# Kernel optimization log

Measured on AMD Instinct MI355X. Metric: run time of the kernel, lower is better.

The kernel has to match this reference:

```python
import jax, jax.numpy as jnp
import numpy as np

TOPK, NUM_CLASSES = 13, 80
ALPHA, BETA, GAMMA, EPS = 1.0, 5.0, 3.0, 1e-09


def _make_boxes(key, shape, img=640.0, wmin=10.0, wmax=120.0):
    k1, k2 = jax.random.split(key)
    cxy = jax.random.uniform(k1, shape[:-1] + (2,), minval=0.0, maxval=img)
    wh = jax.random.uniform(k2, shape[:-1] + (2,), minval=wmin, maxval=wmax)
    return jnp.concatenate([cxy - wh / 2, cxy + wh / 2], axis=-1)


def setup_inputs() -> dict:
    key = jax.random.key(0)
    ks = jax.random.split(key, 7)
    bs, A, C, n = 16, 8400, 80, 60
    return {
        'pd_scores': jax.random.uniform(ks[0], (bs, A, C), dtype=jnp.float32),
        'pd_bboxes': _make_boxes(ks[1], (bs, A, 4)),
        'pd_angles': jax.random.uniform(ks[2], (bs, A, 1), minval=0.0, maxval=90.0),
        'anc_points': jax.random.uniform(ks[3], (A, 2), minval=0.0, maxval=640.0),
        'gt_labels': jax.random.randint(ks[4], (bs, n, 1), 0, C, dtype=jnp.int32),
        'gt_bboxes': _make_boxes(ks[5], (bs, n, 4)),
        'gt_angles': jax.random.uniform(ks[6], (bs, n, 1), minval=0.0, maxval=90.0),
        'mask_gt': jnp.ones((bs, n, 1), jnp.float32),
        'epoch_num': 1,
    }


def _cos_fn(x, ar, beta=2.0):
    return 0.5 + 0.5 * jnp.cos(beta / ar * x / 180.0 * jnp.pi + jnp.pi * (1.0 - beta / (2.0 * ar)))


def _angle_measure(pd_angles, gt_angles, gt_bboxes):
    # gt area ratio w/h -> (bs, n, 1, 1)
    w = gt_bboxes[..., 2:3] - gt_bboxes[..., 0:1]
    h = gt_bboxes[..., 3:4] - gt_bboxes[..., 1:2]
    ar = (w / (h + 1e-05))[:, :, None, :]
    theta = jnp.abs(gt_angles[:, :, None, :] - pd_angles[:, None, :, :])  # (bs,n,A,1)
    av = 1.0 / ar / (2.0 - 1.0 / ar)
    mx = _cos_fn(0.0, ar)
    mn = _cos_fn(90.0, ar)
    r = (_cos_fn(theta, ar) - mn) / (mx - mn) * (1.0 - av) + av
    r = jnp.where(jnp.isnan(r), 0.0, r)
    return jnp.squeeze(r, -1)  # (bs, n, A)


def _pairwise_iou(gt, pd):
    # gt (bs,n,4), pd (bs,A,4) -> (bs,n,A)
    lt = jnp.maximum(gt[:, :, None, :2], pd[:, None, :, :2])
    rb = jnp.minimum(gt[:, :, None, 2:], pd[:, None, :, 2:])
    inter = jnp.clip(rb - lt, 0.0).prod(-1)
    a1 = jnp.clip(gt[..., 2:] - gt[..., :2], 0.0).prod(-1)[:, :, None]
    a2 = jnp.clip(pd[..., 2:] - pd[..., :2], 0.0).prod(-1)[:, None, :]
    return inter / (a1 + a2 - inter + EPS)


def _select_topk(metrics, topk_mask):
    bs, n, A = metrics.shape
    _, idxs = jax.lax.top_k(metrics, TOPK)
    idxs = jnp.where(topk_mask, idxs, 0)
    flat = idxs.reshape(bs * n, TOPK)
    cnt = jnp.zeros((bs * n, A), jnp.int32).at[jnp.arange(bs * n)[:, None], flat].add(1)
    cnt = cnt.reshape(bs, n, A)
    return jnp.where(cnt > 1, 0, cnt).astype(metrics.dtype)


def _select_highest_overlaps(mask_pos, overlaps, n):
    fg = mask_pos.sum(-2)                                   # (bs, A)
    multi = fg[:, None, :] > 1                              # (bs, 1, A)
    is_max = jax.nn.one_hot(overlaps.argmax(1), n, axis=1, dtype=mask_pos.dtype)  # (bs,n,A)
    mask_pos = jnp.where(multi, is_max, mask_pos)
    fg = mask_pos.sum(-2)
    tgt_idx = mask_pos.argmax(-2)                           # (bs, A)
    return tgt_idx, fg, mask_pos


def reference(pd_scores, pd_bboxes, pd_angles, anc_points, gt_labels, gt_bboxes, gt_angles, mask_gt, epoch_num):
    bs, A, C = pd_scores.shape
    n = gt_bboxes.shape[1]
    lab = gt_labels[..., 0].astype(jnp.int32)               # (bs, n)

    # bbox_scores: pd_scores[b, :, gt_label] -> (bs, n, A)
    pts = jnp.transpose(pd_scores, (0, 2, 1))               # (bs, C, A)
    bbox_scores = jnp.take_along_axis(pts, lab[:, :, None], axis=1)

    overlaps = _pairwise_iou(gt_bboxes, pd_bboxes)          # (bs, n, A)
    ang = _angle_measure(pd_angles, gt_angles, gt_bboxes)   # (bs, n, A)
    align = bbox_scores ** ALPHA * overlaps ** BETA * ang ** GAMMA

    # anchors-inside-gt mask (bs, n, A)
    lt = anc_points[None, None, :, :] - gt_bboxes[:, :, None, :2]
    rb = gt_bboxes[:, :, None, 2:] - anc_points[None, None, :, :]
    in_gts = (jnp.concatenate([lt, rb], -1).min(-1) > EPS).astype(align.dtype)

    topk_mask = jnp.broadcast_to(mask_gt > 0, (bs, n, TOPK))
    mask_topk = _select_topk(align * in_gts, topk_mask)
    mask_pos = mask_topk * in_gts * mask_gt                 # (bs, n, A)

    tgt_idx, fg, mask_pos = _select_highest_overlaps(mask_pos, overlaps, n)

    # gather per-anchor targets from flattened gt tensors
    off = tgt_idx + jnp.arange(bs, dtype=tgt_idx.dtype)[:, None] * n   # (bs, A)
    tlab = lab.reshape(-1)[off]
    tlab = jnp.where(tlab < 0, 0, tlab)
    tbb = gt_bboxes.reshape(-1, 4)[off]                     # (bs, A, 4)
    tang = gt_angles.reshape(-1, 1)[off]                    # (bs, A, 1)
    ts = jax.nn.one_hot(tlab, C, dtype=pd_scores.dtype)     # (bs, A, C)
    ts = jnp.where(fg[:, :, None] > 0, ts, 0.0)

    # normalized alignment metric scaling
    align = align * mask_pos
    pam = align.max(-1, keepdims=True)                      # (bs, n, 1)
    pov = (overlaps * mask_pos).max(-1, keepdims=True)      # (bs, n, 1)
    norm = (align * pov / (pam + EPS)).max(-2)[:, :, None]  # (bs, A, 1)
    ts = ts * norm

    return tlab, tbb, tang, ts, fg > 0
```

## Files before the change

### kernel.cpp

```cpp
#include <hip/hip_runtime.h>
#include <math.h>

#define TOPK 13
#define PI_F 3.14159265358979323846f
#define K1_THREADS 256
#define K1_WAVES (K1_THREADS / 64)

typedef unsigned int u32;
typedef unsigned long long u64;

__device__ __forceinline__ u32 ford(float f) {
    u32 u = __float_as_uint(f);
    return (u & 0x80000000u) ? ~u : (u | 0x80000000u);
}
__device__ __forceinline__ float funord(u32 o) {
    u32 u = (o & 0x80000000u) ? (o & 0x7FFFFFFFu) : ~o;
    return __uint_as_float(u);
}

__device__ __forceinline__ float iou_fn(float4 g, float4 p) {
    float ltx = fmaxf(g.x, p.x), lty = fmaxf(g.y, p.y);
    float rbx = fminf(g.z, p.z), rby = fminf(g.w, p.w);
    float inter = fmaxf(rbx - ltx, 0.0f) * fmaxf(rby - lty, 0.0f);
    float a1 = fmaxf(g.z - g.x, 0.0f) * fmaxf(g.w - g.y, 0.0f);
    float a2 = fmaxf(p.z - p.x, 0.0f) * fmaxf(p.w - p.y, 0.0f);
    return inter / (((a1 + a2) - inter) + 1e-9f);
}

struct RowParams { float av, bar, offc, mx, mn; };

__device__ __forceinline__ RowParams row_params(float4 g) {
    float w = g.z - g.x, h = g.w - g.y;
    float ar = w / (h + 1e-5f);
    float ia = 1.0f / ar;
    RowParams rp;
    rp.av = ia / (2.0f - ia);
    rp.bar = 2.0f / ar;
    rp.offc = PI_F * (1.0f - 2.0f / (2.0f * ar));
    rp.mx = 0.5f + 0.5f * cosf(rp.offc);
    rp.mn = 0.5f + 0.5f * cosf(rp.bar * 90.0f / 180.0f * PI_F + rp.offc);
    return rp;
}

__device__ __forceinline__ float ang_measure(const RowParams& rp, float theta) {
    float cfv = 0.5f + 0.5f * cosf(rp.bar * theta / 180.0f * PI_F + rp.offc);
    float r = (cfv - rp.mn) / (rp.mx - rp.mn) * (1.0f - rp.av) + rp.av;
    return isnan(r) ? 0.0f : r;
}

__device__ __forceinline__ float align_fn(float s, float iou, float r) {
    float iou2 = iou * iou;
    float iou5 = (iou2 * iou2) * iou;
    float r3 = (r * r) * r;
    return (s * iou5) * r3;
}

__global__ void k0_init(int* cnt, int* assign1, u32* pam, u32* pov, int BA, int BN) {
    int t = blockIdx.x * blockDim.x + threadIdx.x;
    if (t < BA) { cnt[t] = 0; assign1[t] = -1; }
    if (t < BN) { pam[t] = 0x80000000u; pov[t] = 0x80000000u; }
}

__global__ __launch_bounds__(K1_THREADS)
void k1_topk(const float* __restrict__ scores, const float* __restrict__ pbox,
             const float* __restrict__ pang, const float* __restrict__ anc,
             const int* __restrict__ glab, const float* __restrict__ gbox,
             const float* __restrict__ gang, const float* __restrict__ mgt,
             int* __restrict__ cnt, int* __restrict__ assign1,
             int bs, int A, int n, int C) {
    int j = blockIdx.x;
    int b = j % bs;
    int i = j / bs;
    int bi = b * n + i;
    int tid = threadIdx.x;

    float mg = mgt[bi];
    if (!(mg > 0.0f)) return;

    float4 g = ((const float4*)gbox)[bi];
    int lab = glab[bi];
    float ga = gang[bi];
    RowParams rp = row_params(g);

    const float4* pb = ((const float4*)pbox) + (size_t)b * A;
    const float* pa = pang + (size_t)b * A;
    const float2* ac = (const float2*)anc;
    const float* sc = scores + (size_t)b * A * C + lab;

    u64 arr[TOPK];
#pragma unroll
    for (int jj = 0; jj < TOPK; jj++) arr[jj] = 0ull;
    u64 zkey = 0ull;

    for (int a = tid; a < A; a += K1_THREADS) {
        float4 p = pb[a];
        float pav = pa[a];
        float2 apt = ac[a];
        float iou = iou_fn(g, p);
        float mnv = fminf(fminf(apt.x - g.x, apt.y - g.y), fminf(g.z - apt.x, g.w - apt.y));
        bool needAlign = (mnv > 1e-9f) && (iou > 0.0f);
        if (needAlign || zkey == 0ull) {
            float th = fabsf(ga - pav);
            float r = ang_measure(rp, th);
            bool zeroCand;
            if (needAlign && r > 0.0f) {
                float s = sc[(size_t)a * C];
                float v = align_fn(s, iou, r);
                if (v > 0.0f) {
                    zeroCand = false;
                    u64 key = ((u64)ford(v) << 32) | (u64)(0xFFFFFFFFu - (u32)a);
                    if (key > arr[TOPK - 1]) {
#pragma unroll
                        for (int jj = 0; jj < TOPK; jj++) {
                            u64 hi = arr[jj] > key ? arr[jj] : key;
                            u64 lo = arr[jj] > key ? key : arr[jj];
                            arr[jj] = hi;
                            key = lo;
                        }
                    }
                } else {
                    zeroCand = true;
                }
            } else {
                zeroCand = (r >= 0.0f);
            }
            if (zeroCand && zkey == 0ull) {
                zkey = (0x80000000ull << 32) | (u64)(0xFFFFFFFFu - (u32)a);
            }
        }
    }
    if (zkey > arr[TOPK - 1]) {
        u64 key = zkey;
#pragma unroll
        for (int jj = 0; jj < TOPK; jj++) {
            u64 hi = arr[jj] > key ? arr[jj] : key;
            u64 lo = arr[jj] > key ? key : arr[jj];
            arr[jj] = hi;
            key = lo;
        }
    }

    __shared__ u64 wtop[K1_WAVES * TOPK];
    int lane = tid & 63, wv = tid >> 6;
    for (int round = 0; round < TOPK; round++) {
        u64 m = arr[0];
#pragma unroll
        for (int st = 32; st > 0; st >>= 1) {
            u64 o = __shfl_xor(m, st, 64);
            if (o > m) m = o;
        }
        if (lane == 0) wtop[wv * TOPK + round] = m;
        if (arr[0] == m && m != 0ull) {
#pragma unroll
            for (int jj = 0; jj < TOPK - 1; jj++) arr[jj] = arr[jj + 1];
            arr[TOPK - 1] = 0ull;
        }
    }
    __syncthreads();

    if (wv == 0) {
        const int NK = K1_WAVES * TOPK;
        u64 ka = (lane < NK) ? wtop[lane] : 0ull;
        for (int round = 0; round < TOPK; round++) {
            u64 m = ka;
#pragma unroll
            for (int st = 32; st > 0; st >>= 1) {
                u64 o = __shfl_xor(m, st, 64);
                if (o > m) m = o;
            }
            if (m == 0ull) break;
            if (ka == m) {
                ka = 0ull;
                int a = (int)(0xFFFFFFFFu - (u32)(m & 0xFFFFFFFFull));
                float2 apt = ac[a];
                float mnv = fminf(fminf(apt.x - g.x, apt.y - g.y),
                                  fminf(g.z - apt.x, g.w - apt.y));
                if (mnv > 1e-9f) {
                    atomicAdd(&cnt[(size_t)b * A + a], 1);
                    atomicMax(&assign1[(size_t)b * A + a], i);
                }
            }
        }
    }
}

__global__ __launch_bounds__(256)
void k2_resolve(const float* __restrict__ scores, const float* __restrict__ pbox,
                const float* __restrict__ pang, const int* __restrict__ glab,
                const float* __restrict__ gbox, const float* __restrict__ gang,
                const int* __restrict__ cnt, const int* __restrict__ assign1,
                int* __restrict__ assign, float* __restrict__ alignv,
                u32* __restrict__ pam, u32* __restrict__ pov,
                int bs, int A, int n, int C) {
    int t = blockIdx.x * blockDim.x + threadIdx.x;
    if (t >= bs * A) return;
    int b = t / A;
    int c = cnt[t];
    int asg = -1;
    float alv = 0.0f;
    if (c > 0) {
        float4 p = ((const float4*)pbox)[t];
        if (c == 1) {
            asg = assign1[t];
        } else {
            float best = -1.0f;
            asg = 0;
            for (int i = 0; i < n; i++) {
                float4 gi = ((const float4*)gbox)[b * n + i];
                float io = iou_fn(gi, p);
                if (io > best) { best = io; asg = i; }
            }
        }
        float4 g = ((const float4*)gbox)[b * n + asg];
        RowParams rp = row_params(g);
        float iou = iou_fn(g, p);
        float th = fabsf(gang[b * n + asg] - pang[t]);
        float r = ang_measure(rp, th);
        float s = scores[(size_t)t * C + glab[b * n + asg]];
        alv = align_fn(s, iou, r);
        atomicMax(&pam[b * n + asg], ford(alv));
        atomicMax(&pov[b * n + asg], ford(iou));
    }
    assign[t] = asg;
    alignv[t] = alv;
}

__global__ __launch_bounds__(256)
void k3_out(const int* __restrict__ glab, const float* __restrict__ gbox,
            const float* __restrict__ gang, const int* __restrict__ assign,
            const float* __restrict__ alignv, const u32* __restrict__ pam,
            const u32* __restrict__ pov, float* __restrict__ out,
            int bs, int A, int n, int C) {
    __shared__ float s_nv[256];
    __shared__ int s_lf[256];
    int tid = threadIdx.x;
    int base = blockIdx.x * 256;
    int t = base + tid;
    int BA = bs * A;

    if (t < BA) {
        int b = t / A;
        int asg = assign[t];
        bool fg = asg >= 0;
        int tgt = fg ? asg : 0;
        int lb = glab[b * n + tgt];
        if (lb < 0) lb = 0;

        float* o_tlab = out;
        float* o_tbb = out + BA;
        float* o_tang = out + (size_t)BA * 5;
        float* o_fg = out + (size_t)BA * 6 + (size_t)BA * C;

        o_tlab[t] = (float)lb;
        ((float4*)o_tbb)[t] = ((const float4*)gbox)[b * n + tgt];
        o_tang[t] = gang[b * n + tgt];
        o_fg[t] = fg ? 1.0f : 0.0f;

        float nv = 0.0f;
        if (fg) {
            float pamv = funord(pam[b * n + asg]);
            float povv = funord(pov[b * n + asg]);
            float vv = (alignv[t] * povv) / (pamv + 1e-9f);
            nv = fmaxf(vv, 0.0f);
        }
        s_nv[tid] = nv;
        s_lf[tid] = fg ? lb : -1;
    } else {
        s_nv[tid] = 0.0f;
        s_lf[tid] = -1;
    }
    __syncthreads();

    int Q = C / 4;
    int nA = min(256, BA - base);
    if (nA <= 0) return;
    int total = nA * Q;
    float4* o_ts = (float4*)(out + (size_t)BA * 6) + (size_t)base * Q;
    for (int idx = tid; idx < total; idx += 256) {
        int tl = idx / Q;
        int q = idx - tl * Q;
        float nv = s_nv[tl];
        int lf = s_lf[tl];
        int cb = q * 4;
        float4 o;
        o.x = (lf == cb) ? nv : 0.0f;
        o.y = (lf == cb + 1) ? nv : 0.0f;
        o.z = (lf == cb + 2) ? nv : 0.0f;
        o.w = (lf == cb + 3) ? nv : 0.0f;
        o_ts[idx] = o;
    }
}

extern "C" void kernel_launch(void* const* d_in, const int* in_sizes, int n_in,
                              void* d_out, int out_size, void* d_ws, size_t ws_size,
                              hipStream_t stream) {
    const float* scores = (const float*)d_in[0];
    const float* pbox = (const float*)d_in[1];
    const float* pang = (const float*)d_in[2];
    const float* anc = (const float*)d_in[3];
    const int* glab = (const int*)d_in[4];
    const float* gbox = (const float*)d_in[5];
    const float* gang = (const float*)d_in[6];
    const float* mgt = (const float*)d_in[7];

    const int C = 80;
    int A = in_sizes[3] / 2;
    int bs = in_sizes[0] / (A * C);
    int n = in_sizes[4] / bs;
    int BA = bs * A;
    int BN = bs * n;

    char* ws = (char*)d_ws;
    int* cnt = (int*)ws;        ws += sizeof(int) * (size_t)BA;
    int* assign1 = (int*)ws;    ws += sizeof(int) * (size_t)BA;
    int* assign = (int*)ws;     ws += sizeof(int) * (size_t)BA;
    float* alignv = (float*)ws; ws += sizeof(float) * (size_t)BA;
    u32* pam = (u32*)ws;        ws += sizeof(u32) * (size_t)BN;
    u32* pov = (u32*)ws;        ws += sizeof(u32) * (size_t)BN;

    k0_init<<<(BA + 255) / 256, 256, 0, stream>>>(cnt, assign1, pam, pov, BA, BN);
    k1_topk<<<BN, K1_THREADS, 0, stream>>>(scores, pbox, pang, anc, glab, gbox, gang, mgt,
                                           cnt, assign1, bs, A, n, C);
    k2_resolve<<<(BA + 255) / 256, 256, 0, stream>>>(scores, pbox, pang, glab, gbox, gang,
                                                     cnt, assign1, assign, alignv, pam, pov,
                                                     bs, A, n, C);
    k3_out<<<(BA + 255) / 256, 256, 0, stream>>>(glab, gbox, gang, assign, alignv, pam, pov,
                                                 (float*)d_out, bs, A, n, C);
}
```

Baseline: 170.0 us.

## Split top-k scan into contiguous anchor chunks with separate merge kernel

The per-gt top-k kernel now gives each wavefront a contiguous chunk of anchors (8 chunks, 2 blocks per gt row) instead of striding 256 threads over all anchors. Each wave writes its top-13 list to workspace, and a new 64-thread merge kernel picks the global top-13 and does the atomics. The scan loop also software-prefetches the next anchor's box, angle, anchor point and score. It keeps up to two zero-score candidates per lane so the zero-fill tie-breaking still works after chunking. The cost is an extra kernel launch and a workspace round trip in exchange for more blocks in flight and better memory-latency hiding.

```diff
diff --git a/kernel.cpp b/kernel.cpp
--- a/kernel.cpp
+++ b/kernel.cpp
@@ -3,8 +3,8 @@
 
 #define TOPK 13
 #define PI_F 3.14159265358979323846f
-#define K1_THREADS 256
-#define K1_WAVES (K1_THREADS / 64)
+#define K1_CHUNKS 8
+#define K1_CPB 4
 
 typedef unsigned int u32;
 typedef unsigned long long u64;
@@ -55,27 +55,42 @@
     return (s * iou5) * r3;
 }
 
+__device__ __forceinline__ void insert13(u64* arr, u64 key) {
+    if (key > arr[TOPK - 1]) {
+#pragma unroll
+        for (int jj = 0; jj < TOPK; jj++) {
+            u64 hi = arr[jj] > key ? arr[jj] : key;
+            u64 lo = arr[jj] > key ? key : arr[jj];
+            arr[jj] = hi;
+            key = lo;
+        }
+    }
+}
+
 __global__ void k0_init(int* cnt, int* assign1, u32* pam, u32* pov, int BA, int BN) {
     int t = blockIdx.x * blockDim.x + threadIdx.x;
     if (t < BA) { cnt[t] = 0; assign1[t] = -1; }
     if (t < BN) { pam[t] = 0x80000000u; pov[t] = 0x80000000u; }
 }
 
-__global__ __launch_bounds__(K1_THREADS)
+__global__ __launch_bounds__(256)
 void k1_topk(const float* __restrict__ scores, const float* __restrict__ pbox,
              const float* __restrict__ pang, const float* __restrict__ anc,
              const int* __restrict__ glab, const float* __restrict__ gbox,
              const float* __restrict__ gang, const float* __restrict__ mgt,
-             int* __restrict__ cnt, int* __restrict__ assign1,
+             u64* __restrict__ wslist,
              int bs, int A, int n, int C) {
     int j = blockIdx.x;
     int b = j % bs;
-    int i = j / bs;
+    int r2 = j / bs;
+    int i = r2 % n;
+    int cg = r2 / n;
     int bi = b * n + i;
     int tid = threadIdx.x;
-
-    float mg = mgt[bi];
-    if (!(mg > 0.0f)) return;
+    int lane = tid & 63, wv = tid >> 6;
+    int chunk = cg * K1_CPB + wv;
+
+    if (!(mgt[bi] > 0.0f)) return;
 
     float4 g = ((const float4*)gbox)[bi];
     int lab = glab[bi];
@@ -87,61 +102,69 @@
     const float2* ac = (const float2*)anc;
     const float* sc = scores + (size_t)b * A * C + lab;
 
+    int CS = (A + K1_CHUNKS - 1) / K1_CHUNKS;
+    int start = chunk * CS;
+    int end = min(start + CS, A);
+    int clampA = end - 1;
+
     u64 arr[TOPK];
 #pragma unroll
     for (int jj = 0; jj < TOPK; jj++) arr[jj] = 0ull;
-    u64 zkey = 0ull;
-
-    for (int a = tid; a < A; a += K1_THREADS) {
-        float4 p = pb[a];
-        float pav = pa[a];
-        float2 apt = ac[a];
+    u64 zk0 = 0ull, zk1 = 0ull;
+
+    int a = start + lane;
+    int ca = min(a, clampA);
+    float4 p = pb[ca];
+    float pav = pa[ca];
+    float2 apt = ac[ca];
+    float mnv = fminf(fminf(apt.x - g.x, apt.y - g.y), fminf(g.z - apt.x, g.w - apt.y));
+    bool inG = (mnv > 1e-9f) && (a < end);
+    float s = 0.0f;
+    if (inG) s = sc[(size_t)ca * C];
+
+    int nit = (end - start + 63) >> 6;
+    for (int it = 0; it < nit; ++it) {
+        int an = a + 64;
+        int can = min(an, clampA);
+        float4 p2 = pb[can];
+        float pav2 = pa[can];
+        float2 apt2 = ac[can];
+        float mnv2 = fminf(fminf(apt2.x - g.x, apt2.y - g.y),
+                           fminf(g.z - apt2.x, g.w - apt2.y));
+        bool inG2 = (mnv2 > 1e-9f) && (an < end);
+        float s2 = 0.0f;
+        if (inG2) s2 = sc[(size_t)can * C];
+
         float iou = iou_fn(g, p);
-        float mnv = fminf(fminf(apt.x - g.x, apt.y - g.y), fminf(g.z - apt.x, g.w - apt.y));
-        bool needAlign = (mnv > 1e-9f) && (iou > 0.0f);
-        if (needAlign || zkey == 0ull) {
+        bool needAlign = inG && (iou > 0.0f);
+        bool valid = a < end;
+        if (needAlign || (zk1 == 0ull && valid)) {
             float th = fabsf(ga - pav);
             float r = ang_measure(rp, th);
             bool zeroCand;
             if (needAlign && r > 0.0f) {
-                float s = sc[(size_t)a * C];
                 float v = align_fn(s, iou, r);
                 if (v > 0.0f) {
                     zeroCand = false;
-                    u64 key = ((u64)ford(v) << 32) | (u64)(0xFFFFFFFFu - (u32)a);
-                    if (key > arr[TOPK - 1]) {
-#pragma unroll
-                        for (int jj = 0; jj < TOPK; jj++) {
-                            u64 hi = arr[jj] > key ? arr[jj] : key;
-                            u64 lo = arr[jj] > key ? key : arr[jj];
-                            arr[jj] = hi;
-                            key = lo;
-                        }
-                    }
+                    insert13(arr, ((u64)ford(v) << 32) | (u64)(0xFFFFFFFFu - (u32)a));
                 } else {
                     zeroCand = true;
                 }
             } else {
                 zeroCand = (r >= 0.0f);
             }
-            if (zeroCand && zkey == 0ull) {
-                zkey = (0x80000000ull << 32) | (u64)(0xFFFFFFFFu - (u32)a);
+            if (zeroCand) {
+                u64 kz = (0x80000000ull << 32) | (u64)(0xFFFFFFFFu - (u32)a);
+                if (zk0 == 0ull) zk0 = kz;
+                else if (zk1 == 0ull) zk1 = kz;
             }
         }
-    }
-    if (zkey > arr[TOPK - 1]) {
-        u64 key = zkey;
-#pragma unroll
-        for (int jj = 0; jj < TOPK; jj++) {
-            u64 hi = arr[jj] > key ? arr[jj] : key;
-            u64 lo = arr[jj] > key ? key : arr[jj];
-            arr[jj] = hi;
-            key = lo;
-        }
-    }
-
-    __shared__ u64 wtop[K1_WAVES * TOPK];
-    int lane = tid & 63, wv = tid >> 6;
+        a = an; p = p2; pav = pav2; mnv = mnv2; inG = inG2; s = s2;
+    }
+    insert13(arr, zk0);
+    insert13(arr, zk1);
+
+    u64* dst = wslist + ((size_t)bi * K1_CHUNKS + chunk) * TOPK;
     for (int round = 0; round < TOPK; round++) {
         u64 m = arr[0];
 #pragma unroll
@@ -149,36 +172,54 @@
             u64 o = __shfl_xor(m, st, 64);
             if (o > m) m = o;
         }
-        if (lane == 0) wtop[wv * TOPK + round] = m;
+        if (lane == 0) dst[round] = m;
         if (arr[0] == m && m != 0ull) {
 #pragma unroll
             for (int jj = 0; jj < TOPK - 1; jj++) arr[jj] = arr[jj + 1];
             arr[TOPK - 1] = 0ull;
         }
     }
-    __syncthreads();
-
-    if (wv == 0) {
-        const int NK = K1_WAVES * TOPK;
-        u64 ka = (lane < NK) ? wtop[lane] : 0ull;
-        for (int round = 0; round < TOPK; round++) {
-            u64 m = ka;
-#pragma unroll
-            for (int st = 32; st > 0; st >>= 1) {
-                u64 o = __shfl_xor(m, st, 64);
-                if (o > m) m = o;
-            }
-            if (m == 0ull) break;
-            if (ka == m) {
-                ka = 0ull;
-                int a = (int)(0xFFFFFFFFu - (u32)(m & 0xFFFFFFFFull));
-                float2 apt = ac[a];
-                float mnv = fminf(fminf(apt.x - g.x, apt.y - g.y),
-                                  fminf(g.z - apt.x, g.w - apt.y));
-                if (mnv > 1e-9f) {
-                    atomicAdd(&cnt[(size_t)b * A + a], 1);
-                    atomicMax(&assign1[(size_t)b * A + a], i);
-                }
+}
+
+__global__ __launch_bounds__(64)
+void k1m_merge(const float* __restrict__ anc, const float* __restrict__ gbox,
+               const float* __restrict__ mgt, const u64* __restrict__ wslist,
+               int* __restrict__ cnt, int* __restrict__ assign1,
+               int bs, int A, int n) {
+    int j = blockIdx.x;
+    int b = j % bs;
+    int i = j / bs;
+    int bi = b * n + i;
+    if (!(mgt[bi] > 0.0f)) return;
+    int lane = threadIdx.x;
+
+    const int NK = K1_CHUNKS * TOPK;
+    const u64* src = wslist + (size_t)bi * NK;
+    u64 ka = src[lane];
+    u64 kb = (lane + 64 < NK) ? src[lane + 64] : 0ull;
+
+    float4 g = ((const float4*)gbox)[bi];
+    const float2* ac = (const float2*)anc;
+
+    for (int round = 0; round < TOPK; round++) {
+        u64 m = ka > kb ? ka : kb;
+#pragma unroll
+        for (int st = 32; st > 0; st >>= 1) {
+            u64 o = __shfl_xor(m, st, 64);
+            if (o > m) m = o;
+        }
+        if (m == 0ull) break;
+        bool own = false;
+        if (ka == m) { ka = 0ull; own = true; }
+        else if (kb == m) { kb = 0ull; own = true; }
+        if (own) {
+            int aa = (int)(0xFFFFFFFFu - (u32)(m & 0xFFFFFFFFull));
+            float2 apt = ac[aa];
+            float mnv = fminf(fminf(apt.x - g.x, apt.y - g.y),
+                              fminf(g.z - apt.x, g.w - apt.y));
+            if (mnv > 1e-9f) {
+                atomicAdd(&cnt[(size_t)b * A + aa], 1);
+                atomicMax(&assign1[(size_t)b * A + aa], i);
             }
         }
     }
@@ -311,6 +352,7 @@
     int BN = bs * n;
 
     char* ws = (char*)d_ws;
+    u64* wslist = (u64*)ws;     ws += sizeof(u64) * (size_t)BN * K1_CHUNKS * TOPK;
     int* cnt = (int*)ws;        ws += sizeof(int) * (size_t)BA;
     int* assign1 = (int*)ws;    ws += sizeof(int) * (size_t)BA;
     int* assign = (int*)ws;     ws += sizeof(int) * (size_t)BA;
@@ -319,8 +361,10 @@
     u32* pov = (u32*)ws;        ws += sizeof(u32) * (size_t)BN;
 
     k0_init<<<(BA + 255) / 256, 256, 0, stream>>>(cnt, assign1, pam, pov, BA, BN);
-    k1_topk<<<BN, K1_THREADS, 0, stream>>>(scores, pbox, pang, anc, glab, gbox, gang, mgt,
-                                           cnt, assign1, bs, A, n, C);
+    k1_topk<<<BN * (K1_CHUNKS / K1_CPB), 256, 0, stream>>>(scores, pbox, pang, anc, glab,
+                                                           gbox, gang, mgt, wslist,
+                                                           bs, A, n, C);
+    k1m_merge<<<BN, 64, 0, stream>>>(anc, gbox, mgt, wslist, cnt, assign1, bs, A, n);
     k2_resolve<<<(BA + 255) / 256, 256, 0, stream>>>(scores, pbox, pang, glab, gbox, gang,
                                                      cnt, assign1, assign, alignv, pam, pov,
                                                      bs, A, n, C);
```

Result: slower. 186.9 us (+9.9%).

## Zero the one-hot target buffer inside the top-k kernel and prefetch anchors

Applied to the files above, without the earlier changes.

The large zero-fill of the (bs, A, C) target-score output moves into the top-k kernel. Each block clears its chunk interleaved with its anchor loop, so the memory-bound stores overlap the compute-bound scan. The output kernel then writes only the single nonzero entry per foreground anchor instead of the full dense row. The anchor loop also software-prefetches the next iteration's box, angle and anchor point. The cost is extra store traffic in k1 and a dependency on k1 fully zeroing the buffer before k3 writes into it.

```diff
diff --git a/kernel.cpp b/kernel.cpp
--- a/kernel.cpp
+++ b/kernel.cpp
@@ -3,8 +3,7 @@
 
 #define TOPK 13
 #define PI_F 3.14159265358979323846f
-#define K1_THREADS 256
-#define K1_WAVES (K1_THREADS / 64)
+#define K1_WAVES 4
 
 typedef unsigned int u32;
 typedef unsigned long long u64;
@@ -55,27 +54,51 @@
     return (s * iou5) * r3;
 }
 
+__device__ __forceinline__ void insert13(u64* arr, u64 key) {
+    if (key > arr[TOPK - 1]) {
+#pragma unroll
+        for (int jj = 0; jj < TOPK; jj++) {
+            u64 hi = arr[jj] > key ? arr[jj] : key;
+            u64 lo = arr[jj] > key ? key : arr[jj];
+            arr[jj] = hi;
+            key = lo;
+        }
+    }
+}
+
 __global__ void k0_init(int* cnt, int* assign1, u32* pam, u32* pov, int BA, int BN) {
     int t = blockIdx.x * blockDim.x + threadIdx.x;
     if (t < BA) { cnt[t] = 0; assign1[t] = -1; }
     if (t < BN) { pam[t] = 0x80000000u; pov[t] = 0x80000000u; }
 }
 
-__global__ __launch_bounds__(K1_THREADS)
+__global__ __launch_bounds__(256)
 void k1_topk(const float* __restrict__ scores, const float* __restrict__ pbox,
              const float* __restrict__ pang, const float* __restrict__ anc,
              const int* __restrict__ glab, const float* __restrict__ gbox,
              const float* __restrict__ gang, const float* __restrict__ mgt,
              int* __restrict__ cnt, int* __restrict__ assign1,
+             float* __restrict__ out,
              int bs, int A, int n, int C) {
     int j = blockIdx.x;
     int b = j % bs;
     int i = j / bs;
     int bi = b * n + i;
     int tid = threadIdx.x;
+    int BA = bs * A;
+
+    int nF4 = BA * (C / 4);
+    int zCH = (nF4 + gridDim.x - 1) / gridDim.x;
+    int zBeg = j * zCH + tid;
+    int zEnd = min(j * zCH + zCH, nF4);
+    float4* tsf4 = (float4*)(out + (size_t)BA * 6);
+    const float4 z4 = make_float4(0.0f, 0.0f, 0.0f, 0.0f);
 
     float mg = mgt[bi];
-    if (!(mg > 0.0f)) return;
+    if (!(mg > 0.0f)) {
+        for (; zBeg < zEnd; zBeg += 256) tsf4[zBeg] = z4;
+        return;
+    }
 
     float4 g = ((const float4*)gbox)[bi];
     int lab = glab[bi];
@@ -92,14 +115,28 @@
     for (int jj = 0; jj < TOPK; jj++) arr[jj] = 0ull;
     u64 zkey = 0ull;
 
-    for (int a = tid; a < A; a += K1_THREADS) {
-        float4 p = pb[a];
-        float pav = pa[a];
-        float2 apt = ac[a];
+    int a = tid;
+    float4 p = pb[a];
+    float pav = pa[a];
+    float2 apt = ac[a];
+    float mnv = fminf(fminf(apt.x - g.x, apt.y - g.y), fminf(g.z - apt.x, g.w - apt.y));
+
+    int nit = (A + 255) >> 8;
+    int clampA = A - 1;
+    for (int it = 0; it < nit; ++it) {
+        int an = a + 256;
+        int can = min(an, clampA);
+        float4 p2 = pb[can];
+        float pav2 = pa[can];
+        float2 apt2 = ac[can];
+        if (zBeg < zEnd) { tsf4[zBeg] = z4; zBeg += 256; }
+        float mnv2 = fminf(fminf(apt2.x - g.x, apt2.y - g.y),
+                           fminf(g.z - apt2.x, g.w - apt2.y));
+
+        bool valid = a < A;
         float iou = iou_fn(g, p);
-        float mnv = fminf(fminf(apt.x - g.x, apt.y - g.y), fminf(g.z - apt.x, g.w - apt.y));
-        bool needAlign = (mnv > 1e-9f) && (iou > 0.0f);
-        if (needAlign || zkey == 0ull) {
+        bool needAlign = (mnv > 1e-9f) && (iou > 0.0f) && valid;
+        if (needAlign || (zkey == 0ull && valid)) {
             float th = fabsf(ga - pav);
             float r = ang_measure(rp, th);
             bool zeroCand;
@@ -108,16 +145,7 @@
                 float v = align_fn(s, iou, r);
                 if (v > 0.0f) {
                     zeroCand = false;
-                    u64 key = ((u64)ford(v) << 32) | (u64)(0xFFFFFFFFu - (u32)a);
-                    if (key > arr[TOPK - 1]) {
-#pragma unroll
-                        for (int jj = 0; jj < TOPK; jj++) {
-                            u64 hi = arr[jj] > key ? arr[jj] : key;
-                            u64 lo = arr[jj] > key ? key : arr[jj];
-                            arr[jj] = hi;
-                            key = lo;
-                        }
-                    }
+                    insert13(arr, ((u64)ford(v) << 32) | (u64)(0xFFFFFFFFu - (u32)a));
                 } else {
                     zeroCand = true;
                 }
@@ -128,17 +156,10 @@
                 zkey = (0x80000000ull << 32) | (u64)(0xFFFFFFFFu - (u32)a);
             }
         }
-    }
-    if (zkey > arr[TOPK - 1]) {
-        u64 key = zkey;
-#pragma unroll
-        for (int jj = 0; jj < TOPK; jj++) {
-            u64 hi = arr[jj] > key ? arr[jj] : key;
-            u64 lo = arr[jj] > key ? key : arr[jj];
-            arr[jj] = hi;
-            key = lo;
-        }
-    }
+        a = an; p = p2; pav = pav2; mnv = mnv2;
+    }
+    for (; zBeg < zEnd; zBeg += 256) tsf4[zBeg] = z4;
+    insert13(arr, zkey);
 
     __shared__ u64 wtop[K1_WAVES * TOPK];
     int lane = tid & 63, wv = tid >> 6;
@@ -171,13 +192,13 @@
             if (m == 0ull) break;
             if (ka == m) {
                 ka = 0ull;
-                int a = (int)(0xFFFFFFFFu - (u32)(m & 0xFFFFFFFFull));
-                float2 apt = ac[a];
-                float mnv = fminf(fminf(apt.x - g.x, apt.y - g.y),
-                                  fminf(g.z - apt.x, g.w - apt.y));
-                if (mnv > 1e-9f) {
-                    atomicAdd(&cnt[(size_t)b * A + a], 1);
-                    atomicMax(&assign1[(size_t)b * A + a], i);
+                int aa = (int)(0xFFFFFFFFu - (u32)(m & 0xFFFFFFFFull));
+                float2 ap2 = ac[aa];
+                float mnw = fminf(fminf(ap2.x - g.x, ap2.y - g.y),
+                                  fminf(g.z - ap2.x, g.w - ap2.y));
+                if (mnw > 1e-9f) {
+                    atomicAdd(&cnt[(size_t)b * A + aa], 1);
+                    atomicMax(&assign1[(size_t)b * A + aa], i);
                 }
             }
         }
@@ -231,63 +252,26 @@
             const float* __restrict__ alignv, const u32* __restrict__ pam,
             const u32* __restrict__ pov, float* __restrict__ out,
             int bs, int A, int n, int C) {
-    __shared__ float s_nv[256];
-    __shared__ int s_lf[256];
-    int tid = threadIdx.x;
-    int base = blockIdx.x * 256;
-    int t = base + tid;
+    int t = blockIdx.x * blockDim.x + threadIdx.x;
     int BA = bs * A;
-
-    if (t < BA) {
-        int b = t / A;
-        int asg = assign[t];
-        bool fg = asg >= 0;
-        int tgt = fg ? asg : 0;
-        int lb = glab[b * n + tgt];
-        if (lb < 0) lb = 0;
-
-        float* o_tlab = out;
-        float* o_tbb = out + BA;
-        float* o_tang = out + (size_t)BA * 5;
-        float* o_fg = out + (size_t)BA * 6 + (size_t)BA * C;
-
-        o_tlab[t] = (float)lb;
-        ((float4*)o_tbb)[t] = ((const float4*)gbox)[b * n + tgt];
-        o_tang[t] = gang[b * n + tgt];
-        o_fg[t] = fg ? 1.0f : 0.0f;
-
-        float nv = 0.0f;
-        if (fg) {
-            float pamv = funord(pam[b * n + asg]);
-            float povv = funord(pov[b * n + asg]);
-            float vv = (alignv[t] * povv) / (pamv + 1e-9f);
-            nv = fmaxf(vv, 0.0f);
-        }
-        s_nv[tid] = nv;
-        s_lf[tid] = fg ? lb : -1;
-    } else {
-        s_nv[tid] = 0.0f;
-        s_lf[tid] = -1;
-    }
-    __syncthreads();
-
-    int Q = C / 4;
-    int nA = min(256, BA - base);
-    if (nA <= 0) return;
-    int total = nA * Q;
-    float4* o_ts = (float4*)(out + (size_t)BA * 6) + (size_t)base * Q;
-    for (int idx = tid; idx < total; idx += 256) {
-        int tl = idx / Q;
-        int q = idx - tl * Q;
-        float nv = s_nv[tl];
-        int lf = s_lf[tl];
-        int cb = q * 4;
-        float4 o;
-        o.x = (lf == cb) ? nv : 0.0f;
-        o.y = (lf == cb + 1) ? nv : 0.0f;
-        o.z = (lf == cb + 2) ? nv : 0.0f;
-        o.w = (lf == cb + 3) ? nv : 0.0f;
-        o_ts[idx] = o;
+    if (t >= BA) return;
+    int b = t / A;
+    int asg = assign[t];
+    bool fg = asg >= 0;
+    int tgt = fg ? asg : 0;
+    int lb = glab[b * n + tgt];
+    if (lb < 0) lb = 0;
+
+    out[t] = (float)lb;
+    ((float4*)(out + BA))[t] = ((const float4*)gbox)[b * n + tgt];
+    out[(size_t)BA * 5 + t] = gang[b * n + tgt];
+    out[(size_t)BA * 6 + (size_t)BA * C + t] = fg ? 1.0f : 0.0f;
+
+    if (fg) {
+        float pamv = funord(pam[b * n + asg]);
+        float povv = funord(pov[b * n + asg]);
+        float vv = (alignv[t] * povv) / (pamv + 1e-9f);
+        out[(size_t)BA * 6 + (size_t)t * C + lb] = fmaxf(vv, 0.0f);
     }
 }
 
@@ -319,8 +303,8 @@
     u32* pov = (u32*)ws;        ws += sizeof(u32) * (size_t)BN;
 
     k0_init<<<(BA + 255) / 256, 256, 0, stream>>>(cnt, assign1, pam, pov, BA, BN);
-    k1_topk<<<BN, K1_THREADS, 0, stream>>>(scores, pbox, pang, anc, glab, gbox, gang, mgt,
-                                           cnt, assign1, bs, A, n, C);
+    k1_topk<<<BN, 256, 0, stream>>>(scores, pbox, pang, anc, glab, gbox, gang, mgt,
+                                    cnt, assign1, (float*)d_out, bs, A, n, C);
     k2_resolve<<<(BA + 255) / 256, 256, 0, stream>>>(scores, pbox, pang, glab, gbox, gang,
                                                      cnt, assign1, assign, alignv, pam, pov,
                                                      bs, A, n, C);
```

New measurement: 161.5 us. 1.05x faster.
